# Kernel tuning notes

Measured on AMD Instinct MI355X. Metric: run time of the kernel, lower is better.

## Reference

```python
import jax, jax.numpy as jnp
import numpy as np

B, T, H = 32, 4096, 128   # batch, seq len, feature dim (ctor L=128)
N = 128                    # S5 state size (S5(dim, dim))
DEPTH = 2                  # L_LT
D_OUT = 64                 # adaptive pool output length (ctor D)
LN_EPS = 1e-5


def setup_inputs() -> dict:
    key = jax.random.key(0)
    ks = iter(jax.random.split(key, 40))
    def nrm(shape, s):
        return (jax.random.normal(next(ks), shape, jnp.float32) * s).astype(jnp.float32)
    inp = {}
    inp['x'] = jax.random.normal(next(ks), (B, T, H), jnp.float32)
    # LayerNorm params (stacked over depth)
    inp['ln1_g'] = jnp.ones((DEPTH, H), jnp.float32)
    inp['ln1_b'] = jnp.zeros((DEPTH, H), jnp.float32)
    inp['ln2_g'] = jnp.ones((DEPTH, H), jnp.float32)
    inp['ln2_b'] = jnp.zeros((DEPTH, H), jnp.float32)
    # S5 params: diagonal complex Lambda, complex B/C, real D skip, per-state log step
    inp['Lam_re'] = -0.5 * jnp.ones((DEPTH, N), jnp.float32)
    inp['Lam_im'] = jnp.tile(jnp.pi * jnp.arange(N, dtype=jnp.float32), (DEPTH, 1))
    inp['B_re'] = nrm((DEPTH, N, H), 1.0 / np.sqrt(H))
    inp['B_im'] = nrm((DEPTH, N, H), 1.0 / np.sqrt(H))
    inp['C_re'] = nrm((DEPTH, H, N), 1.0 / np.sqrt(N))
    inp['C_im'] = nrm((DEPTH, H, N), 1.0 / np.sqrt(N))
    inp['D_skip'] = nrm((DEPTH, H), 1.0)
    inp['log_step'] = jax.random.uniform(next(ks), (DEPTH, N), jnp.float32,
                                         minval=np.log(1e-3), maxval=np.log(1e-1))
    # MLP params
    inp['W1'] = nrm((DEPTH, H, 2 * H), 1.0 / np.sqrt(H))
    inp['b1'] = jnp.zeros((DEPTH, 2 * H), jnp.float32)
    inp['W2'] = nrm((DEPTH, 2 * H, H), 1.0 / np.sqrt(2 * H))
    inp['b2'] = jnp.zeros((DEPTH, H), jnp.float32)
    # Conv1d params (out_ch, in_ch, k=5)
    cs = 1.0 / np.sqrt(H * 5)
    inp['conv1_w'] = nrm((H, H, 5), cs)
    inp['conv1_b'] = jnp.zeros((H,), jnp.float32)
    inp['conv2_w'] = nrm((H, H, 5), cs)
    inp['conv2_b'] = jnp.zeros((H,), jnp.float32)
    return inp


def _layer_norm(x, g, b):
    mu = jnp.mean(x, axis=-1, keepdims=True)
    var = jnp.mean(jnp.square(x - mu), axis=-1, keepdims=True)
    return (x - mu) * jax.lax.rsqrt(var + LN_EPS) * g + b


def _s5(u, lam_re, lam_im, b_re, b_im, c_re, c_im, d_skip, log_step):
    # u: [B, T, H] real. Diagonal S5 with ZOH discretization + parallel scan.
    lam = lam_re + 1j * lam_im                       # (N,) complex
    dt = jnp.exp(log_step)                           # (N,)
    lam_bar = jnp.exp(lam * dt)                      # (N,)
    Bc = b_re + 1j * b_im                            # (N, H)
    B_bar = ((lam_bar - 1.0) / lam)[:, None] * Bc    # (N, H)
    Bu = jnp.einsum('bth,nh->btn', u.astype(jnp.complex64), B_bar)  # [B,T,N]
    A = jnp.broadcast_to(lam_bar.astype(jnp.complex64), Bu.shape)
    def binop(e1, e2):
        a1, x1 = e1
        a2, x2 = e2
        return a1 * a2, a2 * x1 + x2
    _, xs = jax.lax.associative_scan(binop, (A, Bu), axis=1)        # [B,T,N]
    Cc = c_re + 1j * c_im                            # (H, N)
    y = 2.0 * jnp.real(jnp.einsum('btn,hn->bth', xs, Cc)) + u * d_skip
    return y


def _conv1d_s2(x, w, b):
    # x: [B, C, L]; stride 2, padding 2, kernel 5
    y = jax.lax.conv_general_dilated(x, w, window_strides=(2,), padding=[(2, 2)],
                                     dimension_numbers=('NCH', 'OIH', 'NCH'))
    return y + b[None, :, None]


def reference(x, ln1_g, ln1_b, ln2_g, ln2_b, Lam_re, Lam_im, B_re, B_im,
              C_re, C_im, D_skip, log_step, W1, b1, W2, b2,
              conv1_w, conv1_b, conv2_w, conv2_b):
    for i in range(DEPTH):
        # S5 sub-block
        res = x
        xn = _layer_norm(x, ln1_g[i], ln1_b[i])
        x = res + _s5(xn, Lam_re[i], Lam_im[i], B_re[i], B_im[i],
                      C_re[i], C_im[i], D_skip[i], log_step[i])
        # MLP sub-block (dropout = identity in eval)
        res = x
        xn = _layer_norm(x, ln2_g[i], ln2_b[i])
        h = jax.nn.gelu(jnp.einsum('bth,hf->btf', xn, W1[i]) + b1[i], approximate=False)
        x = res + jnp.einsum('btf,fh->bth', h, W2[i]) + b2[i]
    x = jnp.transpose(x, (0, 2, 1))                  # [B, H, T]
    x = jax.nn.relu(_conv1d_s2(x, conv1_w, conv1_b))  # [B, H, T/2]
    x = jax.nn.relu(_conv1d_s2(x, conv2_w, conv2_b))  # [B, H, T/4]
    Lin = x.shape[-1]
    # AdaptiveAvgPool1d(D_OUT): Lin divisible by D_OUT -> uniform windows
    x = x.reshape(x.shape[0], x.shape[1], D_OUT, Lin // D_OUT).mean(axis=-1)
    return x  # [B, H, D_OUT]
```

## Files before the change

kernel.cpp:

```cpp
#include <hip/hip_runtime.h>
#include <math.h>

#define BATCH 32
#define TSEQ  4096
#define HD    128
#define NST   128
#define BT    (BATCH*TSEQ)
#define LC    64
#define NCHK  (TSEQ/LC)

typedef unsigned short bf16;
typedef __attribute__((ext_vector_type(8))) short bf16x8;
typedef __attribute__((ext_vector_type(4))) float f32x4;

__device__ __host__ inline int sig_f(int j) {
    return ((j >> 5) << 5) | (((j >> 2) & 3) << 3) | (((j >> 4) & 1) << 2) | (j & 3);
}
__device__ __host__ inline int inv_f(int h) {
    return ((h >> 5) << 5) | (((h >> 2) & 1) << 4) | (((h >> 3) & 3) << 2) | (h & 3);
}

__device__ inline float bf2f(bf16 s) {
    union { unsigned int u; float f; } v; v.u = ((unsigned int)s) << 16; return v.f;
}
__device__ inline bf16 f2bf(float f) {
    union { float f; unsigned int u; } v; v.f = f;
    unsigned int u = v.u;
    unsigned int r = (u + 0x7fffu + ((u >> 16) & 1u)) >> 16;
    return (bf16)r;
}
__device__ inline unsigned int pkpair(float lo, float hi) {
    union { float f; unsigned int u; } a, b;
    a.f = lo; b.f = hi;
    return __builtin_amdgcn_perm(b.u + 0x8000u, a.u + 0x8000u, 0x07060302u);
}
__device__ inline bf16x8 pack8f(float4 f0, float4 f1) {
    union { bf16x8 v; unsigned int u[4]; } t;
    t.u[0] = pkpair(f0.x, f0.y);
    t.u[1] = pkpair(f0.z, f0.w);
    t.u[2] = pkpair(f1.x, f1.y);
    t.u[3] = pkpair(f1.z, f1.w);
    return t.v;
}
__device__ inline float2 cmul2(float2 a, float2 b) {
    return make_float2(a.x*b.x - a.y*b.y, a.x*b.y + a.y*b.x);
}
__device__ inline float gelu_f(float x) {
    float u = x*(0.7978845608f + 0.0356774081f*x*x);
    return __fdividef(x, 1.f + __expf(-2.f*u));
}
__device__ inline float2 upk(unsigned int w) {
    union { unsigned int u; float f; } a, b;
    a.u = w << 16; b.u = w & 0xffff0000u;
    return make_float2(a.f, b.f);
}
__device__ inline unsigned int pk(float2 x) { return pkpair(x.x, x.y); }

__global__ void prep_s5(const float* __restrict__ Lam_re, const float* __restrict__ Lam_im,
                        const float* __restrict__ B_re,  const float* __restrict__ B_im,
                        const float* __restrict__ C_re,  const float* __restrict__ C_im,
                        const float* __restrict__ log_step,
                        const float* __restrict__ ln1_g, const float* __restrict__ ln1_b,
                        const float* __restrict__ D_skip,
                        bf16* __restrict__ Wbu_bf,
                        bf16* __restrict__ Wc_bf,
                        float* __restrict__ Sb, float* __restrict__ biasb,
                        float* __restrict__ gd, float* __restrict__ bd,
                        float4* __restrict__ coefs,
                        float2* __restrict__ apow)
{
    int i = blockIdx.x, n = threadIdx.x;
    int in = i*NST + n;
    float lr = Lam_re[in], li = Lam_im[in];
    float dt = expf(log_step[in]);
    float ea = expf(lr*dt);
    float ar = ea*cosf(li*dt), ai = ea*sinf(li*dt);
    float xx = ar - 1.f, yy = ai;
    float den = lr*lr + li*li;
    float sr = (xx*lr + yy*li)/den;
    float si = (yy*lr - xx*li)/den;
    float2 a2 = make_float2(ar, ai);
    float2 p = a2;
    float2* apr = apow + (size_t)i*64*128;
    for (int j = 0; j < 64; ++j) {
        apr[j*128 + n] = p;
        p = cmul2(p, a2);
    }
    float2 q = a2;
    #pragma unroll
    for (int t = 0; t < 6; ++t) q = cmul2(q, q);
    coefs[in] = make_float4(ar, ai, q.x, q.y);

    const float* g  = ln1_g + i*HD;
    const float* bb = ln1_b + i*HD;
    const float* br = B_re + (size_t)in*HD;
    const float* bi = B_im + (size_t)in*HD;
    bf16* wb = Wbu_bf + (size_t)i*256*128;
    float s_re = 0.f, s_im = 0.f, bc_re = 0.f, bc_im = 0.f;
    for (int h = 0; h < HD; ++h) {
        float wre = sr*br[h] - si*bi[h];
        float wim = sr*bi[h] + si*br[h];
        bf16 wrb = f2bf(g[h]*wre), wib = f2bf(g[h]*wim);
        int hc = (i == 0) ? h : inv_f(h);
        wb[(2*n)*128 + hc]   = wrb;
        wb[(2*n+1)*128 + hc] = wib;
        s_re += bf2f(wrb); s_im += bf2f(wib);
        bc_re += bb[h]*wre; bc_im += bb[h]*wim;
    }
    Sb[i*256 + 2*n] = s_re;     Sb[i*256 + 2*n+1] = s_im;
    biasb[i*256 + 2*n] = bc_re; biasb[i*256 + 2*n+1] = bc_im;

    const float* cr = C_re + (size_t)i*HD*NST;
    const float* ci = C_im + (size_t)i*HD*NST;
    bf16* wc = Wc_bf + (size_t)i*128*256;
    for (int h = 0; h < HD; ++h) {
        int jr = inv_f(h);
        wc[jr*256 + 2*n]   = f2bf( 2.f * cr[h*NST + n]);
        wc[jr*256 + 2*n+1] = f2bf(-2.f * ci[h*NST + n]);
    }
    gd[i*HD + n] = g[n]*D_skip[i*HD + n];
    bd[i*HD + n] = bb[n]*D_skip[i*HD + n];
}

__global__ void prep_w1(const float* __restrict__ W1, const float* __restrict__ b1,
                        const float* __restrict__ ln2_g, const float* __restrict__ ln2_b,
                        bf16* __restrict__ W1_bf, float* __restrict__ S1,
                        float* __restrict__ bias1p)
{
    int i = blockIdx.x, f = threadIdx.x;
    const float* g  = ln2_g + i*HD;
    const float* bb = ln2_b + i*HD;
    bf16* w = W1_bf + (size_t)i*256*128;
    int j = ((f >> 5) << 5) | (((f >> 2) & 1) << 4) | (((f >> 3) & 3) << 2) | (f & 3);
    float S = 0.f, bi_ = b1[i*256 + f];
    for (int h = 0; h < HD; ++h) {
        float wv = W1[(size_t)i*32768 + h*256 + f];
        bf16 wbv = f2bf(g[h]*wv);
        w[j*128 + h] = wbv;
        S += bf2f(wbv);
        bi_ += bb[h]*wv;
    }
    S1[i*256 + f] = S;
    bias1p[i*256 + f] = bi_;
}

__global__ void prep_w2(const float* __restrict__ W2, bf16* __restrict__ W2_bf)
{
    int i = blockIdx.x, h = threadIdx.x;
    bf16* w = W2_bf + (size_t)i*128*256 + (size_t)inv_f(h)*256;
    for (int f = 0; f < 256; ++f)
        w[f] = f2bf(W2[(size_t)i*32768 + f*128 + h]);
}

__global__ void prep_wB(const float* __restrict__ w1, const float* __restrict__ w2,
                        bf16* __restrict__ wB1, bf16* __restrict__ wB2)
{
    int idx = blockIdx.x*256 + threadIdx.x;
    if (idx >= 163840) return;
    int r   = idx % 81920;
    int c   = r / 640;
    int tap = (r % 640) / 128;
    int icj = r % 128;
    if (idx < 81920) {
        wB1[r] = f2bf(w1[(c*128 + sig_f(icj))*5 + tap]);
    } else {
        wB2[r] = f2bf(w2[(c*128 + icj)*5 + tap]);
    }
}

template<typename TA>
__global__ __launch_bounds__(512, 2) void lngemm2(
    const TA* __restrict__ A,
    const bf16* __restrict__ Bt,
    const float* __restrict__ Svec, const float* __restrict__ bvec,
    bf16* __restrict__ outB,
    float2* __restrict__ munrs)
{
    __shared__ bf16 Bs[256*136];
    __shared__ float Sl[256], bl[256];

    int tid = threadIdx.x;
    #pragma unroll
    for (int it = 0; it < 8; ++it) {
        int f = it*512 + tid;
        int n = f >> 4, kk = (f & 15)*8;
        *(bf16x8*)&Bs[n*136 + kk] = *(const bf16x8*)(Bt + n*128 + kk);
    }
    if (tid < 256) { Sl[tid] = Svec[tid]; bl[tid] = bvec[tid]; }
    __syncthreads();

    int wid = tid >> 6, lane = tid & 63;
    int quad = lane >> 4, cl = lane & 15;
    int s0 = blockIdx.x*16 + wid*2;
    size_t row0 = (size_t)s0*16 + cl;

    bf16x8 af[2][4];
    float mu[2], rs[2], mr[2];
    #pragma unroll
    for (int p = 0; p < 2; ++p) {
        size_t row = row0 + (size_t)p*16;
        float sm = 0.f, sq = 0.f;
        if constexpr (sizeof(TA) == 2) {
            const bf16* ar = (const bf16*)A + row*128;
            #pragma unroll
            for (int ks = 0; ks < 4; ++ks) {
                af[p][ks] = *(const bf16x8*)(ar + quad*8 + ks*32);
                union { bf16x8 v; unsigned int u[4]; } aa; aa.v = af[p][ks];
                #pragma unroll
                for (int jp = 0; jp < 4; ++jp) {
                    float2 vv = upk(aa.u[jp]);
                    sm += vv.x + vv.y;
                    sq += vv.x*vv.x + vv.y*vv.y;
                }
            }
        } else {
            const float* ar = (const float*)A + row*128;
            #pragma unroll
            for (int ks = 0; ks < 4; ++ks) {
                float4 f0 = *(const float4*)(ar + quad*8 + ks*32);
                float4 f1 = *(const float4*)(ar + quad*8 + ks*32 + 4);
                sm += f0.x + f0.y + f0.z + f0.w + f1.x + f1.y + f1.z + f1.w;
                sq += f0.x*f0.x + f0.y*f0.y + f0.z*f0.z + f0.w*f0.w
                    + f1.x*f1.x + f1.y*f1.y + f1.z*f1.z + f1.w*f1.w;
                af[p][ks] = pack8f(f0, f1);
            }
        }
        sm += __shfl_xor(sm, 16); sm += __shfl_xor(sm, 32);
        sq += __shfl_xor(sq, 16); sq += __shfl_xor(sq, 32);
        mu[p] = sm * (1.f/128.f);
        rs[p] = rsqrtf(sq*(1.f/128.f) - mu[p]*mu[p] + 1e-5f);
        mr[p] = mu[p]*rs[p];
        if (quad == 0) munrs[row] = make_float2(mu[p], rs[p]);
    }

    #pragma unroll
    for (int g = 0; g < 4; ++g) {
        f32x4 acc0[4] = {}, acc1[4] = {};
        #pragma unroll
        for (int t4 = 0; t4 < 4; ++t4) {
            const bf16* wrp = &Bs[(((g*4+t4)*16) + cl)*136 + quad*8];
            #pragma unroll
            for (int ks = 0; ks < 4; ++ks) {
                bf16x8 w = *(const bf16x8*)(wrp + ks*32);
                acc0[t4] = __builtin_amdgcn_mfma_f32_16x16x32_bf16(w, af[0][ks], acc0[t4], 0, 0, 0);
                acc1[t4] = __builtin_amdgcn_mfma_f32_16x16x32_bf16(w, af[1][ks], acc1[t4], 0, 0, 0);
            }
        }
        #pragma unroll
        for (int t4 = 0; t4 < 4; ++t4) {
            int n0 = (g*4+t4)*16 + quad*4;
            float4 S4 = *(const float4*)&Sl[n0];
            float4 b4 = *(const float4*)&bl[n0];
            float4 o;
            o.x = rs[0]*acc0[t4][0] - mr[0]*S4.x + b4.x;
            o.y = rs[0]*acc0[t4][1] - mr[0]*S4.y + b4.y;
            o.z = rs[0]*acc0[t4][2] - mr[0]*S4.z + b4.z;
            o.w = rs[0]*acc0[t4][3] - mr[0]*S4.w + b4.w;
            *(uint2*)(outB + row0*256 + n0) = make_uint2(pkpair(o.x, o.y), pkpair(o.z, o.w));
            o.x = rs[1]*acc1[t4][0] - mr[1]*S4.x + b4.x;
            o.y = rs[1]*acc1[t4][1] - mr[1]*S4.y + b4.y;
            o.z = rs[1]*acc1[t4][2] - mr[1]*S4.z + b4.z;
            o.w = rs[1]*acc1[t4][3] - mr[1]*S4.w + b4.w;
            *(uint2*)(outB + (row0+16)*256 + n0) = make_uint2(pkpair(o.x, o.y), pkpair(o.z, o.w));
        }
    }
}

template<int FIRST>
__global__ __launch_bounds__(1024, 1) void s5mlp(
    const bf16* __restrict__ A,
    const void* resid,
    bf16* out,
    const float2* __restrict__ munrs,
    const float* __restrict__ gdp, const float* __restrict__ bdp,
    const float2* __restrict__ carry,
    const float2* __restrict__ apow,
    const bf16* __restrict__ Wcp,
    const bf16* __restrict__ W1p,
    const bf16* __restrict__ W2p,
    const float* __restrict__ S1v, const float* __restrict__ b1v,
    const float* __restrict__ b2v)
{
    __shared__ bf16 Xl[128*264];
    __shared__ bf16 Yl[256*132];
    __shared__ float gdl[128], bdl[128], S1l[256], b1l[256], b2l[128];

    int tid = threadIdx.x;
    #pragma unroll
    for (int it = 0; it < 4; ++it) {
        int f = it*1024 + tid;
        int n = f >> 5, kk = (f & 31)*8;
        *(bf16x8*)&Xl[n*264 + kk] = *(const bf16x8*)(Wcp + n*256 + kk);
    }
    #pragma unroll
    for (int it = 0; it < 4; ++it) {
        int f = it*1024 + tid;
        int n = f >> 4, kk = (f & 15)*8;
        *(bf16x8*)&Yl[n*132 + kk] = *(const bf16x8*)(W1p + n*128 + kk);
    }
    if (tid < 128)      { gdl[tid] = gdp[tid]; bdl[tid] = bdp[tid]; }
    else if (tid < 384) { S1l[tid-128] = S1v[tid-128]; b1l[tid-128] = b1v[tid-128]; }
    else if (tid < 512) { b2l[tid-384] = b2v[tid-384]; }
    bf16x8 w2r[4];
    #pragma unroll
    for (int it = 0; it < 4; ++it) {
        int f = it*1024 + tid;
        w2r[it] = *(const bf16x8*)(W2p + (size_t)(f >> 5)*256 + (f & 31)*8);
    }
    __syncthreads();

    int wid = tid >> 6, lane = tid & 63;
    int quad = lane >> 4, cl = lane & 15;
    int s = blockIdx.x*16 + wid;
    size_t row = (size_t)s*16 + cl;

    float2 m2 = munrs[row];
    float mu = m2.x, rs = m2.y;

    bf16x8 af[8];
    {
        const bf16* ar = A + row*256 + quad*8;
        int b  = (int)(row >> 12);
        int tp = (int)(row & 4095);
        int cc = tp >> 6, j = tp & 63;
        const float2* cin = carry + (size_t)cc*(BATCH*NST) + (size_t)b*NST;
        const float2* ap  = apow + (size_t)j*128;
        #pragma unroll
        for (int ks = 0; ks < 8; ++ks) {
            union { bf16x8 v; unsigned int u[4]; } t;
            t.v = *(const bf16x8*)(ar + ks*32);
            int n0c = quad*4 + ks*16;
            #pragma unroll
            for (int jp = 0; jp < 4; ++jp) {
                float2 v  = upk(t.u[jp]);
                float2 ad = cmul2(ap[n0c+jp], cin[n0c+jp]);
                t.u[jp] = pk(make_float2(v.x + ad.x, v.y + ad.y));
            }
            af[ks] = t.v;
        }
    }

    union { unsigned int u[8][2]; bf16x8 v[4]; } hpx;
    #pragma unroll
    for (int nt = 0; nt < 8; ++nt) {
        const bf16* wrp = &Xl[(nt*16 + cl)*264 + quad*8];
        f32x4 a0 = {};
        #pragma unroll
        for (int ks = 0; ks < 8; ++ks)
            a0 = __builtin_amdgcn_mfma_f32_16x16x32_bf16(
                     *(const bf16x8*)(wrp + ks*32), af[ks], a0, 0, 0, 0);
        int fb = ((nt >> 1) << 5) + (quad << 3) + ((nt & 1) << 2);
        float4 rv;
        if constexpr (FIRST) {
            rv = *(const float4*)((const float*)resid + row*128 + fb);
        } else {
            int n0 = nt*16 + quad*4;
            ushort4 u4 = *(const ushort4*)((const bf16*)resid + row*128 + n0);
            rv = make_float4(bf2f(u4.x), bf2f(u4.y), bf2f(u4.z), bf2f(u4.w));
        }
        float4 g4 = *(const float4*)&gdl[fb];
        float4 b4 = *(const float4*)&bdl[fb];
        float4 o;
        o.x = rv.x + a0[0] + (rv.x - mu)*rs*g4.x + b4.x;
        o.y = rv.y + a0[1] + (rv.y - mu)*rs*g4.y + b4.y;
        o.z = rv.z + a0[2] + (rv.z - mu)*rs*g4.z + b4.z;
        o.w = rv.w + a0[3] + (rv.w - mu)*rs*g4.w + b4.w;
        hpx.u[nt][0] = pkpair(o.x, o.y);
        hpx.u[nt][1] = pkpair(o.z, o.w);
    }

    __syncthreads();
    #pragma unroll
    for (int it = 0; it < 4; ++it) {
        int f = it*1024 + tid;
        *(bf16x8*)&Xl[(f >> 5)*264 + (f & 31)*8] = w2r[it];
    }
    __syncthreads();

    float sm = 0.f, sq = 0.f;
    #pragma unroll
    for (int nt = 0; nt < 8; ++nt)
        #pragma unroll
        for (int e = 0; e < 2; ++e) {
            float2 vv = upk(hpx.u[nt][e]);
            sm += vv.x + vv.y;
            sq += vv.x*vv.x + vv.y*vv.y;
        }
    sm += __shfl_xor(sm, 16); sm += __shfl_xor(sm, 32);
    sq += __shfl_xor(sq, 16); sq += __shfl_xor(sq, 32);
    float mu2 = sm * (1.f/128.f);
    float rs2 = rsqrtf(sq*(1.f/128.f) - mu2*mu2 + 1e-5f);
    float mr2 = mu2*rs2;

    union { unsigned int u[16][2]; bf16x8 v[8]; } hp1;
    #pragma unroll
    for (int half = 0; half < 2; ++half) {
        f32x4 acc[8] = {};
        #pragma unroll
        for (int nt = 0; nt < 8; ++nt) {
            const bf16* wrp = &Yl[(((half*8+nt)*16) + cl)*132 + quad*8];
            #pragma unroll
            for (int ks = 0; ks < 4; ++ks)
                acc[nt] = __builtin_amdgcn_mfma_f32_16x16x32_bf16(
                              *(const bf16x8*)(wrp + ks*32), hpx.v[ks], acc[nt], 0, 0, 0);
        }
        #pragma unroll
        for (int nt = 0; nt < 8; ++nt) {
            int NT = half*8 + nt;
            int fb = ((NT >> 1) << 5) + (quad << 3) + ((NT & 1) << 2);
            float4 S4 = *(const float4*)&S1l[fb];
            float4 b4 = *(const float4*)&b1l[fb];
            float4 o;
            o.x = gelu_f(rs2*acc[nt][0] - mr2*S4.x + b4.x);
            o.y = gelu_f(rs2*acc[nt][1] - mr2*S4.y + b4.y);
            o.z = gelu_f(rs2*acc[nt][2] - mr2*S4.z + b4.z);
            o.w = gelu_f(rs2*acc[nt][3] - mr2*S4.w + b4.w);
            hp1.u[NT][0] = pkpair(o.x, o.y);
            hp1.u[NT][1] = pkpair(o.z, o.w);
        }
    }

    #pragma unroll
    for (int nt = 0; nt < 8; ++nt) {
        const bf16* wrp = &Xl[(nt*16 + cl)*264 + quad*8];
        f32x4 a0 = {};
        #pragma unroll
        for (int ks = 0; ks < 8; ++ks)
            a0 = __builtin_amdgcn_mfma_f32_16x16x32_bf16(
                     *(const bf16x8*)(wrp + ks*32), hp1.v[ks], a0, 0, 0, 0);
        int fb = ((nt >> 1) << 5) + (quad << 3) + ((nt & 1) << 2);
        int n0 = nt*16 + quad*4;
        float4 b4 = *(const float4*)&b2l[fb];
        float2 r01 = upk(hpx.u[nt][0]);
        float2 r23 = upk(hpx.u[nt][1]);
        float4 o;
        o.x = a0[0] + b4.x + r01.x;
        o.y = a0[1] + b4.y + r01.y;
        o.z = a0[2] + b4.z + r23.x;
        o.w = a0[3] + b4.w + r23.y;
        *(uint2*)(out + row*128 + n0) = make_uint2(pkpair(o.x, o.y), pkpair(o.z, o.w));
    }
}

__global__ __launch_bounds__(256) void scan_local(unsigned int* __restrict__ xs,
                                                  const float4* __restrict__ coefs,
                                                  float2* __restrict__ carry)
{
    int flat = blockIdx.x*256 + threadIdx.x;
    int n = flat & 127;
    int b = (flat >> 7) & 31;
    int c = flat >> 12;
    float4 cf = coefs[n];
    float2 a = make_float2(cf.x, cf.y);
    unsigned int* base = xs + ((size_t)(b*TSEQ + c*LC))*NST + n;
    float2 x = make_float2(0.f, 0.f);
    for (int j = 0; j < LC; ++j) {
        float2 v = upk(base[(size_t)j*NST]);
        x = make_float2(a.x*x.x - a.y*x.y + v.x, a.x*x.y + a.y*x.x + v.y);
        base[(size_t)j*NST] = pk(x);
    }
    carry[c*(BATCH*NST) + b*NST + n] = x;
}

__global__ void scan_carry(float2* __restrict__ carry, const float4* __restrict__ coefs)
{
    int flat = blockIdx.x*256 + threadIdx.x;
    int n = flat & 127;
    float4 cf = coefs[n];
    float2 aL = make_float2(cf.z, cf.w);
    float2 x = make_float2(0.f, 0.f);
    for (int c = 0; c < NCHK; ++c) {
        float2* p = carry + c*(BATCH*NST) + flat;
        float2 v = *p;
        *p = x;
        x = make_float2(aL.x*x.x - aL.y*x.y + v.x, aL.x*x.y + aL.y*x.x + v.y);
    }
}

__global__ __launch_bounds__(256, 4) void conv1_mfma(
    const bf16* __restrict__ X,
    const bf16* __restrict__ wB,
    const float* __restrict__ bias,
    bf16* __restrict__ out,
    int Tin, int Lout)
{
    __shared__ bf16 As[128][72];
    __shared__ bf16 Bs[128][72];
    int tid  = threadIdx.x;
    int lane = tid & 63;
    int wave = tid >> 6;
    int wm = wave >> 1, wn = wave & 1;
    int quad = lane >> 4, cl = lane & 15;
    int row0 = blockIdx.x * 128;
    int b  = row0 / Lout;
    int l0 = row0 % Lout;
    const bf16* Xb = X + (size_t)b*Tin*128;

    f32x4 acc[4][4] = {};

    for (int k0 = 0; k0 < 640; k0 += 64) {
        int tap = k0 / 128;
        int icb = k0 % 128;
        #pragma unroll
        for (int it = 0; it < 4; ++it) {
            int idx = it*256 + tid;
            int r = idx >> 3, kof = (idx & 7) * 8;
            int t = 2*(l0 + r) - 2 + tap;
            bf16x8 z = {0,0,0,0,0,0,0,0};
            if (t >= 0 && t < Tin) z = *(const bf16x8*)(Xb + (size_t)t*128 + icb + kof);
            *(bf16x8*)&As[r][kof] = z;
        }
        #pragma unroll
        for (int it = 0; it < 4; ++it) {
            int idx = it*256 + tid;
            int n = idx >> 3, kof = (idx & 7) * 8;
            *(bf16x8*)&Bs[n][kof] = *(const bf16x8*)(wB + (size_t)n*640 + k0 + kof);
        }
        __syncthreads();
        #pragma unroll
        for (int kk = 0; kk < 64; kk += 32) {
            bf16x8 af[4], bfr[4];
            #pragma unroll
            for (int i = 0; i < 4; ++i)
                af[i] = *(const bf16x8*)&As[wm*64 + i*16 + cl][kk + quad*8];
            #pragma unroll
            for (int j = 0; j < 4; ++j)
                bfr[j] = *(const bf16x8*)&Bs[wn*64 + j*16 + cl][kk + quad*8];
            #pragma unroll
            for (int i = 0; i < 4; ++i)
                #pragma unroll
                for (int j = 0; j < 4; ++j)
                    acc[i][j] = __builtin_amdgcn_mfma_f32_16x16x32_bf16(
                                    bfr[j], af[i], acc[i][j], 0, 0, 0);
        }
        __syncthreads();
    }

    #pragma unroll
    for (int i = 0; i < 4; ++i) {
        int grow = row0 + wm*64 + i*16 + cl;
        #pragma unroll
        for (int j = 0; j < 4; ++j) {
            int gcol = wn*64 + j*16 + quad*4;
            float4 bv = *(const float4*)(bias + gcol);
            float4 t;
            t.x = fmaxf(acc[i][j][0] + bv.x, 0.f); t.y = fmaxf(acc[i][j][1] + bv.y, 0.f);
            t.z = fmaxf(acc[i][j][2] + bv.z, 0.f); t.w = fmaxf(acc[i][j][3] + bv.w, 0.f);
            uint2 pu = make_uint2(pkpair(t.x, t.y), pkpair(t.z, t.w));
            *(uint2*)(out + (size_t)grow*128 + gcol) = pu;
        }
    }
}

__global__ __launch_bounds__(256, 4) void conv2_pool(
    const bf16* __restrict__ X,
    const bf16* __restrict__ wB,
    const float* __restrict__ bias,
    float* __restrict__ outp,
    int Tin, int Lout)
{
    __shared__ bf16 As[128][72];
    __shared__ bf16 Bs[128][72];
    int tid  = threadIdx.x;
    int lane = tid & 63;
    int wave = tid >> 6;
    int wm = wave >> 1, wn = wave & 1;
    int quad = lane >> 4, cl = lane & 15;
    int row0 = blockIdx.x * 128;
    int b  = row0 / Lout;
    int l0 = row0 % Lout;
    int d0 = l0 / 16;
    const bf16* Xb = X + (size_t)b*Tin*128;

    f32x4 acc[4][4] = {};

    for (int k0 = 0; k0 < 640; k0 += 64) {
        int tap = k0 / 128;
        int icb = k0 % 128;
        #pragma unroll
        for (int it = 0; it < 4; ++it) {
            int idx = it*256 + tid;
            int r = idx >> 3, kof = (idx & 7) * 8;
            int t = 2*(l0 + r) - 2 + tap;
            bf16x8 z = {0,0,0,0,0,0,0,0};
            if (t >= 0 && t < Tin) z = *(const bf16x8*)(Xb + (size_t)t*128 + icb + kof);
            *(bf16x8*)&As[r][kof] = z;
        }
        #pragma unroll
        for (int it = 0; it < 4; ++it) {
            int idx = it*256 + tid;
            int n = idx >> 3, kof = (idx & 7) * 8;
            *(bf16x8*)&Bs[n][kof] = *(const bf16x8*)(wB + (size_t)n*640 + k0 + kof);
        }
        __syncthreads();
        #pragma unroll
        for (int kk = 0; kk < 64; kk += 32) {
            bf16x8 af[4], bfr[4];
            #pragma unroll
            for (int i = 0; i < 4; ++i)
                af[i] = *(const bf16x8*)&As[wm*64 + i*16 + cl][kk + quad*8];
            #pragma unroll
            for (int j = 0; j < 4; ++j)
                bfr[j] = *(const bf16x8*)&Bs[wn*64 + j*16 + cl][kk + quad*8];
            #pragma unroll
            for (int i = 0; i < 4; ++i)
                #pragma unroll
                for (int j = 0; j < 4; ++j)
                    acc[i][j] = __builtin_amdgcn_mfma_f32_16x16x32_bf16(
                                    bfr[j], af[i], acc[i][j], 0, 0, 0);
        }
        __syncthreads();
    }

    #pragma unroll
    for (int j = 0; j < 4; ++j) {
        int gcol = wn*64 + j*16 + quad*4;
        float4 bv = *(const float4*)(bias + gcol);
        #pragma unroll
        for (int i = 0; i < 4; ++i) {
            float4 sp;
            sp.x = fmaxf(acc[i][j][0] + bv.x, 0.f);
            sp.y = fmaxf(acc[i][j][1] + bv.y, 0.f);
            sp.z = fmaxf(acc[i][j][2] + bv.z, 0.f);
            sp.w = fmaxf(acc[i][j][3] + bv.w, 0.f);
            #pragma unroll
            for (int off = 1; off <= 8; off <<= 1) {
                sp.x += __shfl_xor(sp.x, off);
                sp.y += __shfl_xor(sp.y, off);
                sp.z += __shfl_xor(sp.z, off);
                sp.w += __shfl_xor(sp.w, off);
            }
            if (cl == 0) {
                int d = d0 + wm*4 + i;
                float* op = outp + (size_t)b*8192 + (size_t)gcol*64 + d;
                op[0]   = sp.x * (1.f/16.f);
                op[64]  = sp.y * (1.f/16.f);
                op[128] = sp.z * (1.f/16.f);
                op[192] = sp.w * (1.f/16.f);
            }
        }
    }
}

extern "C" void kernel_launch(void* const* d_in, const int* in_sizes, int n_in,
                              void* d_out, int out_size, void* d_ws, size_t ws_size,
                              hipStream_t stream)
{
    (void)in_sizes; (void)n_in; (void)out_size; (void)ws_size;
    const float* x_in    = (const float*)d_in[0];
    const float* ln1_g   = (const float*)d_in[1];
    const float* ln1_b   = (const float*)d_in[2];
    const float* ln2_g   = (const float*)d_in[3];
    const float* ln2_b   = (const float*)d_in[4];
    const float* Lam_re  = (const float*)d_in[5];
    const float* Lam_im  = (const float*)d_in[6];
    const float* B_re    = (const float*)d_in[7];
    const float* B_im    = (const float*)d_in[8];
    const float* C_re    = (const float*)d_in[9];
    const float* C_im    = (const float*)d_in[10];
    const float* D_skip  = (const float*)d_in[11];
    const float* log_step= (const float*)d_in[12];
    const float* W1      = (const float*)d_in[13];
    const float* b1      = (const float*)d_in[14];
    const float* W2      = (const float*)d_in[15];
    const float* b2      = (const float*)d_in[16];
    const float* conv1_w = (const float*)d_in[17];
    const float* conv1_b = (const float*)d_in[18];
    const float* conv2_w = (const float*)d_in[19];
    const float* conv2_b = (const float*)d_in[20];
    float* out = (float*)d_out;

    char* ws = (char*)d_ws;
    bf16*   Xbf    = (bf16*) (ws);
    bf16*   Cbuf   = (bf16*) (ws + (size_t)33554432);
    bf16*   Cv1    = (bf16*) (ws + (size_t)100663296);
    float2* munrs  = (float2*)(ws + (size_t)117440512);
    char*   wreg   = ws + (size_t)118489088;
    bf16*   Wbu_bf = (bf16*)(wreg);
    bf16*   Wc_bf  = (bf16*)(wreg + 131072);
    bf16*   W1_bf  = (bf16*)(wreg + 262144);
    bf16*   W2_bf  = (bf16*)(wreg + 393216);
    float*  Sb     = (float*)(wreg + 524288);
    float*  biasb  = (float*)(wreg + 526336);
    float*  S1     = (float*)(wreg + 528384);
    float*  bias1p = (float*)(wreg + 530432);
    float*  gd     = (float*)(wreg + 532480);
    float*  bd     = (float*)(wreg + 533504);
    float4* coefs  = (float4*)(wreg + 534528);
    bf16*   wB1    = (bf16*)(wreg + 538624);
    bf16*   wB2    = (bf16*)(wreg + 702464);
    float2* carry  = (float2*)(wreg + 866304);
    float2* apow   = (float2*)(wreg + 2963456);

    prep_s5<<<2, 128, 0, stream>>>(Lam_re, Lam_im, B_re, B_im, C_re, C_im, log_step,
                                   ln1_g, ln1_b, D_skip,
                                   Wbu_bf, Wc_bf, Sb, biasb, gd, bd, coefs, apow);
    prep_w1<<<2, 256, 0, stream>>>(W1, b1, ln2_g, ln2_b, W1_bf, S1, bias1p);
    prep_w2<<<2, 128, 0, stream>>>(W2, W2_bf);
    prep_wB<<<640, 256, 0, stream>>>(conv1_w, conv2_w, wB1, wB2);

    for (int i = 0; i < 2; ++i) {
        if (i == 0)
            lngemm2<float><<<512, 512, 0, stream>>>(
                x_in, Wbu_bf, Sb, biasb, Cbuf, munrs);
        else
            lngemm2<bf16><<<512, 512, 0, stream>>>(
                Xbf, Wbu_bf + 32768, Sb + 256, biasb + 256, Cbuf, munrs);
        scan_local<<<1024, 256, 0, stream>>>((unsigned int*)Cbuf, coefs + i*NST, carry);
        scan_carry<<<16, 256, 0, stream>>>(carry, coefs + i*NST);
        if (i == 0)
            s5mlp<1><<<512, 1024, 0, stream>>>(
                Cbuf, x_in, Xbf, munrs, gd, bd, carry, apow,
                Wc_bf, W1_bf, W2_bf, S1, bias1p, b2);
        else
            s5mlp<0><<<512, 1024, 0, stream>>>(
                Cbuf, Xbf, Xbf, munrs, gd + 128, bd + 128, carry, apow + 64*128,
                Wc_bf + 32768, W1_bf + 32768, W2_bf + 32768,
                S1 + 256, bias1p + 256, b2 + 128);
    }

    conv1_mfma<<<512, 256, 0, stream>>>(Xbf, wB1, conv1_b, Cv1, 4096, 2048);
    conv2_pool<<<256, 256, 0, stream>>>(Cv1, wB2, conv2_b, out, 2048, 1024);
}
```

Measured before the change: 632.9 us.

## Restructure s5mlp for two blocks per CU and widen scan_local to two states per thread

s5mlp no longer keeps the W2 weights in registers across the first GEMM. It now loads them after the first LayerNorm/residual stage and writes them to shared memory between the MLP GEMMs. Launch bounds change to allow two 1024-thread blocks per CU, and the MFMA accumulators are batched before the epilogues. scan_local now processes two complex states per thread with 64-bit loads, halving the grid. The risks are register spilling under the tighter bound, and shared memory (~100KB per block) may still block a second resident block. The W2 load latency is now exposed mid-kernel, and the scan has fewer threads in flight.

```diff
diff --git a/kernel.cpp b/kernel.cpp
--- a/kernel.cpp
+++ b/kernel.cpp
@@ -267,7 +267,7 @@
 }
 
 template<int FIRST>
-__global__ __launch_bounds__(1024, 1) void s5mlp(
+__global__ __launch_bounds__(1024, 2) void s5mlp(
     const bf16* __restrict__ A,
     const void* resid,
     bf16* out,
@@ -301,12 +301,6 @@
     if (tid < 128)      { gdl[tid] = gdp[tid]; bdl[tid] = bdp[tid]; }
     else if (tid < 384) { S1l[tid-128] = S1v[tid-128]; b1l[tid-128] = b1v[tid-128]; }
     else if (tid < 512) { b2l[tid-384] = b2v[tid-384]; }
-    bf16x8 w2r[4];
-    #pragma unroll
-    for (int it = 0; it < 4; ++it) {
-        int f = it*1024 + tid;
-        w2r[it] = *(const bf16x8*)(W2p + (size_t)(f >> 5)*256 + (f & 31)*8);
-    }
     __syncthreads();
 
     int wid = tid >> 6, lane = tid & 63;
@@ -340,15 +334,18 @@
         }
     }
 
-    union { unsigned int u[8][2]; bf16x8 v[4]; } hpx;
+    f32x4 accA[8] = {};
     #pragma unroll
     for (int nt = 0; nt < 8; ++nt) {
         const bf16* wrp = &Xl[(nt*16 + cl)*264 + quad*8];
-        f32x4 a0 = {};
         #pragma unroll
         for (int ks = 0; ks < 8; ++ks)
-            a0 = __builtin_amdgcn_mfma_f32_16x16x32_bf16(
-                     *(const bf16x8*)(wrp + ks*32), af[ks], a0, 0, 0, 0);
+            accA[nt] = __builtin_amdgcn_mfma_f32_16x16x32_bf16(
+                           *(const bf16x8*)(wrp + ks*32), af[ks], accA[nt], 0, 0, 0);
+    }
+    union { unsigned int u[8][2]; bf16x8 v[4]; } hpx;
+    #pragma unroll
+    for (int nt = 0; nt < 8; ++nt) {
         int fb = ((nt >> 1) << 5) + (quad << 3) + ((nt & 1) << 2);
         float4 rv;
         if constexpr (FIRST) {
@@ -361,21 +358,24 @@
         float4 g4 = *(const float4*)&gdl[fb];
         float4 b4 = *(const float4*)&bdl[fb];
         float4 o;
-        o.x = rv.x + a0[0] + (rv.x - mu)*rs*g4.x + b4.x;
-        o.y = rv.y + a0[1] + (rv.y - mu)*rs*g4.y + b4.y;
-        o.z = rv.z + a0[2] + (rv.z - mu)*rs*g4.z + b4.z;
-        o.w = rv.w + a0[3] + (rv.w - mu)*rs*g4.w + b4.w;
+        o.x = rv.x + accA[nt][0] + (rv.x - mu)*rs*g4.x + b4.x;
+        o.y = rv.y + accA[nt][1] + (rv.y - mu)*rs*g4.y + b4.y;
+        o.z = rv.z + accA[nt][2] + (rv.z - mu)*rs*g4.z + b4.z;
+        o.w = rv.w + accA[nt][3] + (rv.w - mu)*rs*g4.w + b4.w;
         hpx.u[nt][0] = pkpair(o.x, o.y);
         hpx.u[nt][1] = pkpair(o.z, o.w);
     }
 
     __syncthreads();
-    #pragma unroll
-    for (int it = 0; it < 4; ++it) {
-        int f = it*1024 + tid;
-        *(bf16x8*)&Xl[(f >> 5)*264 + (f & 31)*8] = w2r[it];
-    }
-    __syncthreads();
+
+    bf16x8 w2a, w2b, w2c, w2d;
+    {
+        int f0 = tid, f1 = 1024 + tid, f2 = 2048 + tid, f3 = 3072 + tid;
+        w2a = *(const bf16x8*)(W2p + (size_t)(f0 >> 5)*256 + (f0 & 31)*8);
+        w2b = *(const bf16x8*)(W2p + (size_t)(f1 >> 5)*256 + (f1 & 31)*8);
+        w2c = *(const bf16x8*)(W2p + (size_t)(f2 >> 5)*256 + (f2 & 31)*8);
+        w2d = *(const bf16x8*)(W2p + (size_t)(f3 >> 5)*256 + (f3 & 31)*8);
+    }
 
     float sm = 0.f, sq = 0.f;
     #pragma unroll
@@ -391,6 +391,14 @@
     float mu2 = sm * (1.f/128.f);
     float rs2 = rsqrtf(sq*(1.f/128.f) - mu2*mu2 + 1e-5f);
     float mr2 = mu2*rs2;
+
+    {
+        int f0 = tid, f1 = 1024 + tid, f2 = 2048 + tid, f3 = 3072 + tid;
+        *(bf16x8*)&Xl[(f0 >> 5)*264 + (f0 & 31)*8] = w2a;
+        *(bf16x8*)&Xl[(f1 >> 5)*264 + (f1 & 31)*8] = w2b;
+        *(bf16x8*)&Xl[(f2 >> 5)*264 + (f2 & 31)*8] = w2c;
+        *(bf16x8*)&Xl[(f3 >> 5)*264 + (f3 & 31)*8] = w2d;
+    }
 
     union { unsigned int u[16][2]; bf16x8 v[8]; } hp1;
     #pragma unroll
@@ -420,46 +428,55 @@
         }
     }
 
+    __syncthreads();
+
+    f32x4 accC[8] = {};
     #pragma unroll
     for (int nt = 0; nt < 8; ++nt) {
         const bf16* wrp = &Xl[(nt*16 + cl)*264 + quad*8];
-        f32x4 a0 = {};
         #pragma unroll
         for (int ks = 0; ks < 8; ++ks)
-            a0 = __builtin_amdgcn_mfma_f32_16x16x32_bf16(
-                     *(const bf16x8*)(wrp + ks*32), hp1.v[ks], a0, 0, 0, 0);
+            accC[nt] = __builtin_amdgcn_mfma_f32_16x16x32_bf16(
+                           *(const bf16x8*)(wrp + ks*32), hp1.v[ks], accC[nt], 0, 0, 0);
+    }
+    #pragma unroll
+    for (int nt = 0; nt < 8; ++nt) {
         int fb = ((nt >> 1) << 5) + (quad << 3) + ((nt & 1) << 2);
         int n0 = nt*16 + quad*4;
         float4 b4 = *(const float4*)&b2l[fb];
         float2 r01 = upk(hpx.u[nt][0]);
         float2 r23 = upk(hpx.u[nt][1]);
         float4 o;
-        o.x = a0[0] + b4.x + r01.x;
-        o.y = a0[1] + b4.y + r01.y;
-        o.z = a0[2] + b4.z + r23.x;
-        o.w = a0[3] + b4.w + r23.y;
+        o.x = accC[nt][0] + b4.x + r01.x;
+        o.y = accC[nt][1] + b4.y + r01.y;
+        o.z = accC[nt][2] + b4.z + r23.x;
+        o.w = accC[nt][3] + b4.w + r23.y;
         *(uint2*)(out + row*128 + n0) = make_uint2(pkpair(o.x, o.y), pkpair(o.z, o.w));
     }
 }
 
-__global__ __launch_bounds__(256) void scan_local(unsigned int* __restrict__ xs,
+__global__ __launch_bounds__(256) void scan_local(uint2* __restrict__ xs,
                                                   const float4* __restrict__ coefs,
                                                   float2* __restrict__ carry)
 {
     int flat = blockIdx.x*256 + threadIdx.x;
-    int n = flat & 127;
-    int b = (flat >> 7) & 31;
-    int c = flat >> 12;
-    float4 cf = coefs[n];
-    float2 a = make_float2(cf.x, cf.y);
-    unsigned int* base = xs + ((size_t)(b*TSEQ + c*LC))*NST + n;
-    float2 x = make_float2(0.f, 0.f);
+    int n2 = flat & 63;
+    int b = (flat >> 6) & 31;
+    int c = flat >> 11;
+    float4 cf0 = coefs[2*n2], cf1 = coefs[2*n2+1];
+    float2 a0 = make_float2(cf0.x, cf0.y);
+    float2 a1 = make_float2(cf1.x, cf1.y);
+    uint2* base = xs + ((size_t)(b*TSEQ + c*LC))*64 + n2;
+    float2 x0 = make_float2(0.f, 0.f), x1 = make_float2(0.f, 0.f);
     for (int j = 0; j < LC; ++j) {
-        float2 v = upk(base[(size_t)j*NST]);
-        x = make_float2(a.x*x.x - a.y*x.y + v.x, a.x*x.y + a.y*x.x + v.y);
-        base[(size_t)j*NST] = pk(x);
-    }
-    carry[c*(BATCH*NST) + b*NST + n] = x;
+        uint2 v = base[(size_t)j*64];
+        float2 v0 = upk(v.x), v1 = upk(v.y);
+        x0 = make_float2(a0.x*x0.x - a0.y*x0.y + v0.x, a0.x*x0.y + a0.y*x0.x + v0.y);
+        x1 = make_float2(a1.x*x1.x - a1.y*x1.y + v1.x, a1.x*x1.y + a1.y*x1.x + v1.y);
+        base[(size_t)j*64] = make_uint2(pk(x0), pk(x1));
+    }
+    carry[c*(BATCH*NST) + b*NST + 2*n2]   = x0;
+    carry[c*(BATCH*NST) + b*NST + 2*n2+1] = x1;
 }
 
 __global__ void scan_carry(float2* __restrict__ carry, const float4* __restrict__ coefs)
@@ -706,7 +723,7 @@
         else
             lngemm2<bf16><<<512, 512, 0, stream>>>(
                 Xbf, Wbu_bf + 32768, Sb + 256, biasb + 256, Cbuf, munrs);
-        scan_local<<<1024, 256, 0, stream>>>((unsigned int*)Cbuf, coefs + i*NST, carry);
+        scan_local<<<512, 256, 0, stream>>>((uint2*)Cbuf, coefs + i*NST, carry);
         scan_carry<<<16, 256, 0, stream>>>(carry, coefs + i*NST);
         if (i == 0)
             s5mlp<1><<<512, 1024, 0, stream>>>(
```

New measurement: 630.8 us. No clear change (-0.3%).

## Halve s5mlp block size for two blocks per CU and vectorize scan_local

Applied to the files above, without the earlier changes.

The fused S5+MLP kernel now runs 512-thread blocks with launch bounds allowing two blocks per CU, where it previously ran one 1024-thread block. The W2 weights are loaded into registers after the first GEMM and written to shared memory before the W1 GEMM, with the barrier moved after the GELU stage. The first MLP GEMM is restructured to accumulate one tile at a time, which reduces live accumulators and register pressure. scan_local now processes two state channels per thread with 8-byte loads and stores, halving its thread count. These changes aim to raise occupancy and overlap, and to widen memory accesses in the scan. The risk is that shared memory per block (~135KB) may not actually fit two blocks per CU, and that each block now reloads the full weight set for half as many rows.

```diff
diff --git a/kernel.cpp b/kernel.cpp
--- a/kernel.cpp
+++ b/kernel.cpp
@@ -267,7 +267,7 @@
 }
 
 template<int FIRST>
-__global__ __launch_bounds__(1024, 1) void s5mlp(
+__global__ __launch_bounds__(512, 2) void s5mlp(
     const bf16* __restrict__ A,
     const void* resid,
     bf16* out,
@@ -287,31 +287,25 @@
 
     int tid = threadIdx.x;
     #pragma unroll
-    for (int it = 0; it < 4; ++it) {
-        int f = it*1024 + tid;
+    for (int it = 0; it < 8; ++it) {
+        int f = it*512 + tid;
         int n = f >> 5, kk = (f & 31)*8;
         *(bf16x8*)&Xl[n*264 + kk] = *(const bf16x8*)(Wcp + n*256 + kk);
     }
     #pragma unroll
-    for (int it = 0; it < 4; ++it) {
-        int f = it*1024 + tid;
+    for (int it = 0; it < 8; ++it) {
+        int f = it*512 + tid;
         int n = f >> 4, kk = (f & 15)*8;
         *(bf16x8*)&Yl[n*132 + kk] = *(const bf16x8*)(W1p + n*128 + kk);
     }
     if (tid < 128)      { gdl[tid] = gdp[tid]; bdl[tid] = bdp[tid]; }
     else if (tid < 384) { S1l[tid-128] = S1v[tid-128]; b1l[tid-128] = b1v[tid-128]; }
-    else if (tid < 512) { b2l[tid-384] = b2v[tid-384]; }
-    bf16x8 w2r[4];
-    #pragma unroll
-    for (int it = 0; it < 4; ++it) {
-        int f = it*1024 + tid;
-        w2r[it] = *(const bf16x8*)(W2p + (size_t)(f >> 5)*256 + (f & 31)*8);
-    }
+    else                { b2l[tid-384] = b2v[tid-384]; }
     __syncthreads();
 
     int wid = tid >> 6, lane = tid & 63;
     int quad = lane >> 4, cl = lane & 15;
-    int s = blockIdx.x*16 + wid;
+    int s = blockIdx.x*8 + wid;
     size_t row = (size_t)s*16 + cl;
 
     float2 m2 = munrs[row];
@@ -370,12 +364,13 @@
     }
 
     __syncthreads();
-    #pragma unroll
-    for (int it = 0; it < 4; ++it) {
-        int f = it*1024 + tid;
-        *(bf16x8*)&Xl[(f >> 5)*264 + (f & 31)*8] = w2r[it];
-    }
-    __syncthreads();
+
+    bf16x8 w2r[8];
+    #pragma unroll
+    for (int it = 0; it < 8; ++it) {
+        int f = it*512 + tid;
+        w2r[it] = *(const bf16x8*)(W2p + (size_t)(f >> 5)*256 + (f & 31)*8);
+    }
 
     float sm = 0.f, sq = 0.f;
     #pragma unroll
@@ -392,33 +387,38 @@
     float rs2 = rsqrtf(sq*(1.f/128.f) - mu2*mu2 + 1e-5f);
     float mr2 = mu2*rs2;
 
+    #pragma unroll
+    for (int it = 0; it < 8; ++it) {
+        int f = it*512 + tid;
+        *(bf16x8*)&Xl[(f >> 5)*264 + (f & 31)*8] = w2r[it];
+    }
+
     union { unsigned int u[16][2]; bf16x8 v[8]; } hp1;
     #pragma unroll
     for (int half = 0; half < 2; ++half) {
-        f32x4 acc[8] = {};
-        #pragma unroll
-        for (int nt = 0; nt < 8; ++nt) {
-            const bf16* wrp = &Yl[(((half*8+nt)*16) + cl)*132 + quad*8];
-            #pragma unroll
-            for (int ks = 0; ks < 4; ++ks)
-                acc[nt] = __builtin_amdgcn_mfma_f32_16x16x32_bf16(
-                              *(const bf16x8*)(wrp + ks*32), hpx.v[ks], acc[nt], 0, 0, 0);
-        }
         #pragma unroll
         for (int nt = 0; nt < 8; ++nt) {
             int NT = half*8 + nt;
+            const bf16* wrp = &Yl[((NT*16) + cl)*132 + quad*8];
+            f32x4 a0 = {};
+            #pragma unroll
+            for (int ks = 0; ks < 4; ++ks)
+                a0 = __builtin_amdgcn_mfma_f32_16x16x32_bf16(
+                         *(const bf16x8*)(wrp + ks*32), hpx.v[ks], a0, 0, 0, 0);
             int fb = ((NT >> 1) << 5) + (quad << 3) + ((NT & 1) << 2);
             float4 S4 = *(const float4*)&S1l[fb];
             float4 b4 = *(const float4*)&b1l[fb];
             float4 o;
-            o.x = gelu_f(rs2*acc[nt][0] - mr2*S4.x + b4.x);
-            o.y = gelu_f(rs2*acc[nt][1] - mr2*S4.y + b4.y);
-            o.z = gelu_f(rs2*acc[nt][2] - mr2*S4.z + b4.z);
-            o.w = gelu_f(rs2*acc[nt][3] - mr2*S4.w + b4.w);
+            o.x = gelu_f(rs2*a0[0] - mr2*S4.x + b4.x);
+            o.y = gelu_f(rs2*a0[1] - mr2*S4.y + b4.y);
+            o.z = gelu_f(rs2*a0[2] - mr2*S4.z + b4.z);
+            o.w = gelu_f(rs2*a0[3] - mr2*S4.w + b4.w);
             hp1.u[NT][0] = pkpair(o.x, o.y);
             hp1.u[NT][1] = pkpair(o.z, o.w);
         }
     }
+
+    __syncthreads();
 
     #pragma unroll
     for (int nt = 0; nt < 8; ++nt) {
@@ -442,24 +442,28 @@
     }
 }
 
-__global__ __launch_bounds__(256) void scan_local(unsigned int* __restrict__ xs,
+__global__ __launch_bounds__(256) void scan_local(uint2* __restrict__ xs,
                                                   const float4* __restrict__ coefs,
                                                   float2* __restrict__ carry)
 {
     int flat = blockIdx.x*256 + threadIdx.x;
-    int n = flat & 127;
-    int b = (flat >> 7) & 31;
-    int c = flat >> 12;
-    float4 cf = coefs[n];
-    float2 a = make_float2(cf.x, cf.y);
-    unsigned int* base = xs + ((size_t)(b*TSEQ + c*LC))*NST + n;
-    float2 x = make_float2(0.f, 0.f);
+    int n2 = flat & 63;
+    int b = (flat >> 6) & 31;
+    int c = flat >> 11;
+    float4 cf0 = coefs[2*n2], cf1 = coefs[2*n2+1];
+    float2 a0 = make_float2(cf0.x, cf0.y);
+    float2 a1 = make_float2(cf1.x, cf1.y);
+    uint2* base = xs + ((size_t)(b*TSEQ + c*LC))*64 + n2;
+    float2 x0 = make_float2(0.f, 0.f), x1 = make_float2(0.f, 0.f);
     for (int j = 0; j < LC; ++j) {
-        float2 v = upk(base[(size_t)j*NST]);
-        x = make_float2(a.x*x.x - a.y*x.y + v.x, a.x*x.y + a.y*x.x + v.y);
-        base[(size_t)j*NST] = pk(x);
-    }
-    carry[c*(BATCH*NST) + b*NST + n] = x;
+        uint2 v = base[(size_t)j*64];
+        float2 v0 = upk(v.x), v1 = upk(v.y);
+        x0 = make_float2(a0.x*x0.x - a0.y*x0.y + v0.x, a0.x*x0.y + a0.y*x0.x + v0.y);
+        x1 = make_float2(a1.x*x1.x - a1.y*x1.y + v1.x, a1.x*x1.y + a1.y*x1.x + v1.y);
+        base[(size_t)j*64] = make_uint2(pk(x0), pk(x1));
+    }
+    carry[c*(BATCH*NST) + b*NST + 2*n2]   = x0;
+    carry[c*(BATCH*NST) + b*NST + 2*n2+1] = x1;
 }
 
 __global__ void scan_carry(float2* __restrict__ carry, const float4* __restrict__ coefs)
@@ -706,14 +710,14 @@
         else
             lngemm2<bf16><<<512, 512, 0, stream>>>(
                 Xbf, Wbu_bf + 32768, Sb + 256, biasb + 256, Cbuf, munrs);
-        scan_local<<<1024, 256, 0, stream>>>((unsigned int*)Cbuf, coefs + i*NST, carry);
+        scan_local<<<512, 256, 0, stream>>>((uint2*)Cbuf, coefs + i*NST, carry);
         scan_carry<<<16, 256, 0, stream>>>(carry, coefs + i*NST);
         if (i == 0)
-            s5mlp<1><<<512, 1024, 0, stream>>>(
+            s5mlp<1><<<1024, 512, 0, stream>>>(
                 Cbuf, x_in, Xbf, munrs, gd, bd, carry, apow,
                 Wc_bf, W1_bf, W2_bf, S1, bias1p, b2);
         else
-            s5mlp<0><<<512, 1024, 0, stream>>>(
+            s5mlp<0><<<1024, 512, 0, stream>>>(
                 Cbuf, Xbf, Xbf, munrs, gd + 128, bd + 128, carry, apow + 64*128,
                 Wc_bf + 32768, W1_bf + 32768, W2_bf + 32768,
                 S1 + 256, bias1p + 256, b2 + 128);
```

After: 635.7 us. Within noise of the previous version (+0.4%).
